# Optimization experiments

Hardware: AMD Instinct MI355X
Metric: run time of the kernel (lower is better)

## Reference

```python
import jax, jax.numpy as jnp
import numpy as np

DIM = 256
N_HEADS = 4
B, N = 2, 4096


def setup_inputs() -> dict:
    key = jax.random.key(0)
    ks = jax.random.split(key, 10)
    s = DIM ** -0.5
    return {
        "x": jax.random.normal(ks[0], (B, N, DIM), dtype=jnp.float32),
        "q_w": jax.random.normal(ks[1], (DIM, DIM), dtype=jnp.float32) * s,
        "q_b": jnp.zeros((DIM,), dtype=jnp.float32),
        "k_w": jax.random.normal(ks[2], (DIM, DIM), dtype=jnp.float32) * s,
        "k_b": jnp.zeros((DIM,), dtype=jnp.float32),
        "v_w": jax.random.normal(ks[3], (DIM, DIM), dtype=jnp.float32) * s,
        "v_b": jnp.zeros((DIM,), dtype=jnp.float32),
        "o_w": jax.random.normal(ks[4], (DIM, DIM), dtype=jnp.float32) * s,
        "o_b": jnp.zeros((DIM,), dtype=jnp.float32),
        "tau": jnp.ones((1,), dtype=jnp.float32),
    }


def reference(x, q_w, q_b, k_w, k_b, v_w, v_b, o_w, o_b, tau):
    Bsz, Nlen, C = x.shape
    H = N_HEADS
    Dh = C // H
    scale = C ** -0.5  # source uses full dim, not head_dim
    Q = (x @ q_w.T + q_b).reshape(Bsz, Nlen, H, Dh)
    K = (x @ k_w.T + k_b).reshape(Bsz, Nlen, H, Dh)
    V = (x @ v_w.T + v_b).reshape(Bsz, Nlen, H, Dh)
    attn = jnp.einsum('bnhd,bmhd->bhnm', Q, K) * scale
    # soft-threshold gate: keep only |attn| > tau, then relu
    attn = jax.nn.relu(jnp.where(jnp.abs(attn) > tau, attn, 0.0))
    attn = jax.nn.softmax(attn, axis=-1)
    out = jnp.einsum('bhnm,bmhd->bnhd', attn, V).reshape(Bsz, Nlen, C)
    return out @ o_w.T + o_b
```

## Files before the change

### kernel.cpp

```cpp
#include <hip/hip_runtime.h>

#define SEQ   4096
#define CDIM  256
#define NHEAD 4
#define DHEAD 64
#define PSTRIDE 72

typedef float    f32x4 __attribute__((ext_vector_type(4)));
typedef _Float16 f16x8 __attribute__((ext_vector_type(8)));
typedef _Float16 f16x4 __attribute__((ext_vector_type(4)));

__device__ __forceinline__ f16x8 cvt_frag(const float* __restrict__ p) {
    float4 f0 = *(const float4*)p;
    float4 f1 = *(const float4*)(p + 4);
    f16x8 r;
    r[0]=(_Float16)f0.x; r[1]=(_Float16)f0.y; r[2]=(_Float16)f0.z; r[3]=(_Float16)f0.w;
    r[4]=(_Float16)f1.x; r[5]=(_Float16)f1.y; r[6]=(_Float16)f1.z; r[7]=(_Float16)f1.w;
    return r;
}

__global__ __launch_bounds__(256) void sta_prep(
    const float* __restrict__ qw, const float* __restrict__ kw,
    const float* __restrict__ vw, const float* __restrict__ ow,
    _Float16* __restrict__ w16)
{
    const int mat = blockIdx.y;
    const float* src = (mat == 0) ? qw : (mat == 1) ? kw : (mat == 2) ? vw : ow;
    const int i = (blockIdx.x * 256 + threadIdx.x) * 8;
    *(f16x8*)(w16 + mat * 65536 + i) = cvt_frag(src + i);
}

__global__ __launch_bounds__(256) void sta_qkv(
    const float* __restrict__ x, const _Float16* __restrict__ w16,
    const float* __restrict__ qb, const float* __restrict__ kb, const float* __restrict__ vb,
    _Float16* __restrict__ Qo, _Float16* __restrict__ Ko, _Float16* __restrict__ Vo)
{
    const int wave = threadIdx.x >> 6;
    const int lane = threadIdx.x & 63;
    const int l15  = lane & 15;
    const int quad = lane >> 4;
    const int mat  = blockIdx.y;
    const int half = blockIdx.z;
    const int row0 = blockIdx.x * 64 + wave * 16;

    const _Float16* w    = w16 + mat * 65536;
    const float*    bias = (mat == 0) ? qb : (mat == 1) ? kb : vb;

    f16x8 xf[8];
    const float* xrow = x + (row0 + l15) * CDIM + quad * 8;
    #pragma unroll
    for (int ks = 0; ks < 8; ks++) xf[ks] = cvt_frag(xrow + ks * 32);

    #pragma unroll 1
    for (int ct = 0; ct < 8; ct++) {
        const int ctg = half * 8 + ct;
        const _Float16* wr = w + (ctg * 16 + l15) * CDIM + quad * 8;
        f32x4 acc = {0.f, 0.f, 0.f, 0.f};
        if (mat < 2) {
            #pragma unroll
            for (int ks = 0; ks < 8; ks++)
                acc = __builtin_amdgcn_mfma_f32_16x16x32_f16(*(const f16x8*)(wr + ks * 32), xf[ks], acc, 0, 0, 0);
            const float4 bv = *(const float4*)(bias + ctg * 16 + quad * 4);
            const int c0 = ctg * 16 + quad * 4;
            const int h = c0 >> 6, d0 = c0 & 63;
            const int grow = row0 + l15, b = grow >> 12, n = grow & (SEQ - 1);
            const float sc = (mat == 0) ? 0.0625f : 1.0f;
            f16x4 o;
            o[0] = (_Float16)((acc[0] + bv.x) * sc);
            o[1] = (_Float16)((acc[1] + bv.y) * sc);
            o[2] = (_Float16)((acc[2] + bv.z) * sc);
            o[3] = (_Float16)((acc[3] + bv.w) * sc);
            _Float16* dst = ((mat == 0) ? Qo : Ko) + (((b * NHEAD + h) * SEQ + n) * DHEAD + d0);
            *(f16x4*)dst = o;
        } else {
            #pragma unroll
            for (int ks = 0; ks < 8; ks++)
                acc = __builtin_amdgcn_mfma_f32_16x16x32_f16(xf[ks], *(const f16x8*)(wr + ks * 32), acc, 0, 0, 0);
            const int c = ctg * 16 + l15;
            const int h = c >> 6, d = c & 63;
            const float bv = bias[c];
            const int grow0 = row0 + quad * 4, b = grow0 >> 12, n0 = grow0 & (SEQ - 1);
            f16x4 o;
            #pragma unroll
            for (int r = 0; r < 4; r++) o[r] = (_Float16)(acc[r] + bv);
            *(f16x4*)(Vo + (((b * NHEAD + h) * DHEAD + d) * SEQ + n0)) = o;
        }
    }
}

__global__ __launch_bounds__(64) void sta_attn(
    const _Float16* __restrict__ Q, const _Float16* __restrict__ K, const _Float16* __restrict__ Vt,
    const float* __restrict__ taup,
    float* __restrict__ Opart, float* __restrict__ lpart)
{
    __shared__ __align__(16) _Float16 pbuf[64 * PSTRIDE];

    const int lane = threadIdx.x;
    const int l15  = lane & 15;
    const int quad = lane >> 4;
    const int qt = blockIdx.x;
    const int bh = blockIdx.y;
    const int sp = blockIdx.z;
    const float tau_eff = fmaxf(taup[0], 0.0f);

    const _Float16* Qb = Q  + bh * SEQ * DHEAD;
    const _Float16* Kb = K  + bh * SEQ * DHEAD;
    const _Float16* Vb = Vt + bh * DHEAD * SEQ;

    const int q0 = qt * 64;

    f16x8 qf[4][2];
    #pragma unroll
    for (int qb = 0; qb < 4; qb++)
        #pragma unroll
        for (int ks = 0; ks < 2; ks++)
            qf[qb][ks] = *(const f16x8*)(Qb + (q0 + qb * 16 + l15) * DHEAD + ks * 32 + quad * 8);

    f32x4 O[4][4];
    #pragma unroll
    for (int qb = 0; qb < 4; qb++)
        #pragma unroll
        for (int db = 0; db < 4; db++) O[qb][db] = (f32x4){0.f, 0.f, 0.f, 0.f};
    float rs[4] = {0.f, 0.f, 0.f, 0.f};

    #pragma unroll 1
    for (int kt = sp * 16; kt < sp * 16 + 16; kt++) {
        const int kv0 = kt * 64;

        #pragma unroll
        for (int kb = 0; kb < 4; kb++) {
            const _Float16* kp = Kb + (kv0 + kb * 16 + l15) * DHEAD + quad * 8;
            f16x8 k0 = *(const f16x8*)kp;
            f16x8 k1 = *(const f16x8*)(kp + 32);
            #pragma unroll
            for (int qb = 0; qb < 4; qb++) {
                f32x4 a = {0.f, 0.f, 0.f, 0.f};
                a = __builtin_amdgcn_mfma_f32_16x16x32_f16(k0, qf[qb][0], a, 0, 0, 0);
                a = __builtin_amdgcn_mfma_f32_16x16x32_f16(k1, qf[qb][1], a, 0, 0, 0);
                f16x4 pk;
                float acc = 0.f;
                #pragma unroll
                for (int r = 0; r < 4; r++) {
                    float e = __expf(a[r]);
                    float p = (a[r] > tau_eff) ? e : 1.0f;
                    acc += p;
                    pk[r] = (_Float16)p;
                }
                rs[qb] += acc;
                *(f16x4*)(pbuf + (qb * 16 + l15) * PSTRIDE + kb * 16 + quad * 4) = pk;
            }
        }

        #pragma unroll
        for (int ks = 0; ks < 2; ks++) {
            f16x8 pa[4];
            #pragma unroll
            for (int qb = 0; qb < 4; qb++)
                pa[qb] = *(const f16x8*)(pbuf + (qb * 16 + l15) * PSTRIDE + ks * 32 + quad * 8);
            #pragma unroll
            for (int db = 0; db < 4; db++) {
                f16x8 vf = *(const f16x8*)(Vb + (db * 16 + l15) * SEQ + kv0 + ks * 32 + quad * 8);
                #pragma unroll
                for (int qb = 0; qb < 4; qb++)
                    O[qb][db] = __builtin_amdgcn_mfma_f32_16x16x32_f16(pa[qb], vf, O[qb][db], 0, 0, 0);
            }
        }
    }

    #pragma unroll
    for (int qb = 0; qb < 4; qb++) {
        float v = rs[qb];
        v += __shfl_xor(v, 16);
        v += __shfl_xor(v, 32);
        rs[qb] = v;
    }
    float* Ob = Opart + (size_t)((sp * 8 + bh) * SEQ + q0) * DHEAD;
    #pragma unroll
    for (int qb = 0; qb < 4; qb++)
        #pragma unroll
        for (int db = 0; db < 4; db++)
            #pragma unroll
            for (int r = 0; r < 4; r++)
                Ob[(qb * 16 + quad * 4 + r) * DHEAD + db * 16 + l15] = O[qb][db][r];
    if (quad == 0) {
        #pragma unroll
        for (int qb = 0; qb < 4; qb++)
            lpart[(sp * 8 + bh) * SEQ + q0 + qb * 16 + l15] = rs[qb];
    }
}

__global__ __launch_bounds__(256) void sta_combine(
    const float* __restrict__ Opart, const float* __restrict__ lpart,
    _Float16* __restrict__ AO)
{
    const int idx = blockIdx.x * 256 + threadIdx.x;
    const int dg = idx & 15, n = (idx >> 4) & (SEQ - 1), bh = idx >> 16;
    const int d0 = dg * 4;
    float4 o = {0.f, 0.f, 0.f, 0.f};
    float l = 0.f;
    #pragma unroll
    for (int s = 0; s < 4; s++) {
        const float4 os = *(const float4*)(Opart + (size_t)((s * 8 + bh) * SEQ + n) * DHEAD + d0);
        o.x += os.x; o.y += os.y; o.z += os.z; o.w += os.w;
        l += lpart[(s * 8 + bh) * SEQ + n];
    }
    const float inv = 1.0f / l;
    const int b = bh >> 2, h = bh & 3;
    f16x4 res;
    res[0] = (_Float16)(o.x * inv); res[1] = (_Float16)(o.y * inv);
    res[2] = (_Float16)(o.z * inv); res[3] = (_Float16)(o.w * inv);
    *(f16x4*)(AO + (size_t)(b * SEQ + n) * CDIM + h * DHEAD + d0) = res;
}

__global__ __launch_bounds__(256) void sta_oproj(
    const _Float16* __restrict__ AO, const _Float16* __restrict__ w16o,
    const float* __restrict__ ob, float* __restrict__ out)
{
    const int wave = threadIdx.x >> 6;
    const int lane = threadIdx.x & 63;
    const int l15  = lane & 15;
    const int quad = lane >> 4;
    const int row0 = blockIdx.x * 64 + wave * 16;
    const int quarter = blockIdx.y;

    f16x8 af[8];
    const _Float16* arow = AO + (row0 + l15) * CDIM + quad * 8;
    #pragma unroll
    for (int ks = 0; ks < 8; ks++) af[ks] = *(const f16x8*)(arow + ks * 32);

    #pragma unroll 1
    for (int ct = 0; ct < 4; ct++) {
        const int ctg = quarter * 4 + ct;
        const _Float16* wr = w16o + (ctg * 16 + l15) * CDIM + quad * 8;
        f32x4 acc = {0.f, 0.f, 0.f, 0.f};
        #pragma unroll
        for (int ks = 0; ks < 8; ks++)
            acc = __builtin_amdgcn_mfma_f32_16x16x32_f16(*(const f16x8*)(wr + ks * 32), af[ks], acc, 0, 0, 0);
        const float4 bv = *(const float4*)(ob + ctg * 16 + quad * 4);
        const int c0 = ctg * 16 + quad * 4;
        float4 res;
        res.x = acc[0] + bv.x; res.y = acc[1] + bv.y;
        res.z = acc[2] + bv.z; res.w = acc[3] + bv.w;
        *(float4*)(out + (size_t)(row0 + l15) * CDIM + c0) = res;
    }
}

extern "C" void kernel_launch(void* const* d_in, const int* in_sizes, int n_in,
                              void* d_out, int out_size, void* d_ws, size_t ws_size,
                              hipStream_t stream) {
    const float* x   = (const float*)d_in[0];
    const float* qw  = (const float*)d_in[1];
    const float* qb  = (const float*)d_in[2];
    const float* kw  = (const float*)d_in[3];
    const float* kb  = (const float*)d_in[4];
    const float* vw  = (const float*)d_in[5];
    const float* vb  = (const float*)d_in[6];
    const float* ow  = (const float*)d_in[7];
    const float* ob  = (const float*)d_in[8];
    const float* tau = (const float*)d_in[9];

    _Float16* w16 = (_Float16*)d_ws;
    _Float16* Q   = w16 + 262144;
    _Float16* K   = Q + 2097152;
    _Float16* Vt  = K + 2097152;
    _Float16* AO  = Vt + 2097152;
    float* Opart  = (float*)(AO + 2097152);
    float* lpart  = Opart + 8388608;

    sta_prep   <<<dim3(32, 4),      256, 0, stream>>>(qw, kw, vw, ow, w16);
    sta_qkv    <<<dim3(128, 3, 2),  256, 0, stream>>>(x, w16, qb, kb, vb, Q, K, Vt);
    sta_attn   <<<dim3(64, 8, 4),    64, 0, stream>>>(Q, K, Vt, tau, Opart, lpart);
    sta_combine<<<2048,             256, 0, stream>>>(Opart, lpart, AO);
    sta_oproj  <<<dim3(128, 4),     256, 0, stream>>>(AO, ow ? (w16 + 3 * 65536) : (w16 + 3 * 65536), ob, (float*)d_out);
}
```

Before: 208.4 us.

## Split attention KV range across two waves per block with LDS reduction

Each attention block now runs two waves. Each wave handles half of the block's 16 KV tiles, using its own LDS P buffer. After the loop, the two waves exchange partial O and row sums through LDS, and each wave writes half of the query rows. This doubles the number of concurrent waves and halves the serial loop length per wave, in exchange for a cross-wave reduction and two barriers. It also drops a redundant ternary in the oproj launch.

```diff
diff --git a/kernel.cpp b/kernel.cpp
--- a/kernel.cpp
+++ b/kernel.cpp
@@ -88,14 +88,15 @@
     }
 }
 
-__global__ __launch_bounds__(64) void sta_attn(
+__global__ __launch_bounds__(128, 4) void sta_attn(
     const _Float16* __restrict__ Q, const _Float16* __restrict__ K, const _Float16* __restrict__ Vt,
     const float* __restrict__ taup,
     float* __restrict__ Opart, float* __restrict__ lpart)
 {
-    __shared__ __align__(16) _Float16 pbuf[64 * PSTRIDE];
-
-    const int lane = threadIdx.x;
+    __shared__ __align__(16) _Float16 pbuf[2 * 64 * PSTRIDE];
+
+    const int wave = threadIdx.x >> 6;
+    const int lane = threadIdx.x & 63;
     const int l15  = lane & 15;
     const int quad = lane >> 4;
     const int qt = blockIdx.x;
@@ -103,6 +104,8 @@
     const int sp = blockIdx.z;
     const float tau_eff = fmaxf(taup[0], 0.0f);
 
+    _Float16* pb = pbuf + wave * (64 * PSTRIDE);
+
     const _Float16* Qb = Q  + bh * SEQ * DHEAD;
     const _Float16* Kb = K  + bh * SEQ * DHEAD;
     const _Float16* Vb = Vt + bh * DHEAD * SEQ;
@@ -123,8 +126,9 @@
         for (int db = 0; db < 4; db++) O[qb][db] = (f32x4){0.f, 0.f, 0.f, 0.f};
     float rs[4] = {0.f, 0.f, 0.f, 0.f};
 
+    const int kt0 = sp * 16 + wave * 8;
     #pragma unroll 1
-    for (int kt = sp * 16; kt < sp * 16 + 16; kt++) {
+    for (int kt = kt0; kt < kt0 + 8; kt++) {
         const int kv0 = kt * 64;
 
         #pragma unroll
@@ -147,7 +151,7 @@
                     pk[r] = (_Float16)p;
                 }
                 rs[qb] += acc;
-                *(f16x4*)(pbuf + (qb * 16 + l15) * PSTRIDE + kb * 16 + quad * 4) = pk;
+                *(f16x4*)(pb + (qb * 16 + l15) * PSTRIDE + kb * 16 + quad * 4) = pk;
             }
         }
 
@@ -156,7 +160,7 @@
             f16x8 pa[4];
             #pragma unroll
             for (int qb = 0; qb < 4; qb++)
-                pa[qb] = *(const f16x8*)(pbuf + (qb * 16 + l15) * PSTRIDE + ks * 32 + quad * 8);
+                pa[qb] = *(const f16x8*)(pb + (qb * 16 + l15) * PSTRIDE + ks * 32 + quad * 8);
             #pragma unroll
             for (int db = 0; db < 4; db++) {
                 f16x8 vf = *(const f16x8*)(Vb + (db * 16 + l15) * SEQ + kv0 + ks * 32 + quad * 8);
@@ -167,8 +171,34 @@
         }
     }
 
-    #pragma unroll
-    for (int qb = 0; qb < 4; qb++) {
+    __syncthreads();
+    const int oth = 1 - wave;
+    float* xw = (float*)(pbuf + wave * (64 * PSTRIDE));
+    #pragma unroll
+    for (int qh = 0; qh < 2; qh++) {
+        const int qb = oth * 2 + qh;
+        #pragma unroll
+        for (int db = 0; db < 4; db++)
+            *(f32x4*)(xw + (qh * 4 + db) * 256 + lane * 4) = O[qb][db];
+        xw[2048 + qh * 64 + lane] = rs[qb];
+    }
+    __syncthreads();
+    const float* xr = (const float*)(pbuf + oth * (64 * PSTRIDE));
+    #pragma unroll
+    for (int qh = 0; qh < 2; qh++) {
+        const int qb = wave * 2 + qh;
+        #pragma unroll
+        for (int db = 0; db < 4; db++) {
+            f32x4 t = *(const f32x4*)(xr + (qh * 4 + db) * 256 + lane * 4);
+            O[qb][db][0] += t[0]; O[qb][db][1] += t[1];
+            O[qb][db][2] += t[2]; O[qb][db][3] += t[3];
+        }
+        rs[qb] += xr[2048 + qh * 64 + lane];
+    }
+
+    #pragma unroll
+    for (int qh = 0; qh < 2; qh++) {
+        const int qb = wave * 2 + qh;
         float v = rs[qb];
         v += __shfl_xor(v, 16);
         v += __shfl_xor(v, 32);
@@ -176,16 +206,20 @@
     }
     float* Ob = Opart + (size_t)((sp * 8 + bh) * SEQ + q0) * DHEAD;
     #pragma unroll
-    for (int qb = 0; qb < 4; qb++)
+    for (int qh = 0; qh < 2; qh++) {
+        const int qb = wave * 2 + qh;
         #pragma unroll
         for (int db = 0; db < 4; db++)
             #pragma unroll
             for (int r = 0; r < 4; r++)
                 Ob[(qb * 16 + quad * 4 + r) * DHEAD + db * 16 + l15] = O[qb][db][r];
+    }
     if (quad == 0) {
         #pragma unroll
-        for (int qb = 0; qb < 4; qb++)
+        for (int qh = 0; qh < 2; qh++) {
+            const int qb = wave * 2 + qh;
             lpart[(sp * 8 + bh) * SEQ + q0 + qb * 16 + l15] = rs[qb];
+        }
     }
 }
 
@@ -269,7 +303,7 @@
 
     sta_prep   <<<dim3(32, 4),      256, 0, stream>>>(qw, kw, vw, ow, w16);
     sta_qkv    <<<dim3(128, 3, 2),  256, 0, stream>>>(x, w16, qb, kb, vb, Q, K, Vt);
-    sta_attn   <<<dim3(64, 8, 4),    64, 0, stream>>>(Q, K, Vt, tau, Opart, lpart);
+    sta_attn   <<<dim3(64, 8, 4),   128, 0, stream>>>(Q, K, Vt, tau, Opart, lpart);
     sta_combine<<<2048,             256, 0, stream>>>(Opart, lpart, AO);
-    sta_oproj  <<<dim3(128, 4),     256, 0, stream>>>(AO, ow ? (w16 + 3 * 65536) : (w16 + 3 * 65536), ob, (float*)d_out);
-}
+    sta_oproj  <<<dim3(128, 4),     256, 0, stream>>>(AO, w16 + 3 * 65536, ob, (float*)d_out);
+}
```

New measurement: 428.2 us. 105% more time.
